# Optimization experiments

Measured on AMD Instinct MI355X. Metric: run time of the kernel, lower is better.

Reference implementation:

```python
import jax, jax.numpy as jnp
import numpy as np

B, N, D = 32, 65536, 16
M, H, OUT = 32, 64, 3  # m_model_output, hidden width, i_model output


def setup_inputs() -> dict:
    key = jax.random.key(0)
    ks = jax.random.split(key, 5)
    s = lambda fan_in: 1.0 / np.sqrt(fan_in)
    return {
        "inputs": jax.random.normal(ks[0], (B, N, D), dtype=jnp.float32),
        "mw1": jax.random.normal(ks[1], (D, H), dtype=jnp.float32) * s(D),
        "mb1": jnp.zeros((H,), dtype=jnp.float32),
        "mw2": jax.random.normal(ks[2], (H, M), dtype=jnp.float32) * s(H),
        "mb2": jnp.zeros((M,), dtype=jnp.float32),
        "iw1": jax.random.normal(ks[3], (M + 1, H), dtype=jnp.float32) * s(M + 1),
        "ib1": jnp.zeros((H,), dtype=jnp.float32),
        "iw2": jax.random.normal(ks[4], (H, OUT), dtype=jnp.float32) * s(H),
        "ib2": jnp.zeros((OUT,), dtype=jnp.float32),
    }


def reference(inputs, mw1, mb1, mw2, mb2, iw1, ib1, iw2, ib2):
    # m_model: per-node MLP producing messages [B, N, M]
    h = jax.nn.relu(jnp.einsum("bnd,dh->bnh", inputs, mw1) + mb1)
    messages = jnp.einsum("bnh,hm->bnm", h, mw2) + mb2
    # concat(messages[:j], messages[j:]) is identity -> sum over ALL nodes
    msg_sum = jnp.sum(messages, axis=1, keepdims=True)  # [B, 1, M]
    msg_sum = jnp.broadcast_to(msg_sum, (inputs.shape[0], inputs.shape[1], messages.shape[-1]))
    # append each node's last scalar feature -> [B, N, M+1]
    feat = jnp.concatenate([msg_sum, inputs[..., -1:]], axis=-1)
    # i_model: per-node MLP -> [B, N, OUT]
    g = jax.nn.relu(jnp.einsum("bnf,fh->bnh", feat, iw1) + ib1)
    out = jnp.einsum("bnh,ho->bno", g, iw2) + ib2
    return out
```

## Files before the change

### kernel.cpp

```cpp
#include <hip/hip_runtime.h>
#include <hip/hip_bf16.h>

#define Bb   32
#define Nn   65536
#define Dd   16
#define Hh   64
#define Mm   32
#define OUTn 3

#define TPB    256
#define CHUNK  256
#define NCH    8
#define SEGN   (CHUNK * NCH)
#define NWAVES ((Bb * Nn) / 512)
#define WPB    (NWAVES / Bb)
#define NSEG   65

typedef __attribute__((ext_vector_type(8)))  __bf16 bf16x8;
typedef __attribute__((ext_vector_type(4)))  __bf16 bf16x4;
typedef __attribute__((ext_vector_type(16))) float  f32x16;
typedef __attribute__((ext_vector_type(4)))  float  f32x4;

static __device__ inline void split_bf(float w, __bf16& hi, __bf16& lo) {
    hi = (__bf16)w;
    lo = (__bf16)(w - (float)hi);
}

typedef const __attribute__((address_space(1))) unsigned int gu32;
typedef __attribute__((address_space(3))) unsigned int lu32;
static __device__ __forceinline__ void gld16(const float* g, float* l) {
    __builtin_amdgcn_global_load_lds((gu32*)g, (lu32*)l, 16, 0, 0);
}

__global__ __launch_bounds__(TPB) void k_mphase(
    const float* __restrict__ in, const float* __restrict__ mw1,
    const float* __restrict__ mb1, float* __restrict__ partials,
    __bf16* __restrict__ xlast)
{
    __shared__ float lds[2][CHUNK * Dd];

    const int tid  = threadIdx.x;
    const int lane = tid & 63;
    const int w    = tid >> 6;
    const int l31  = lane & 31;
    const int half = lane >> 5;
    const size_t blk0 = (size_t)blockIdx.x * SEGN;

    bf16x8 bhiA, bloA, bhiB, bloB;
#pragma unroll
    for (int e = 0; e < 8; ++e) {
        const int k = 8 * half + e;
        __bf16 h, l;
        split_bf(mw1[k * Hh + l31], h, l);        bhiA[e] = h; bloA[e] = l;
        split_bf(mw1[k * Hh + 32 + l31], h, l);   bhiB[e] = h; bloB[e] = l;
    }
    const float biasA = mb1[l31];
    const float biasB = mb1[32 + l31];

    float hsumA = 0.f, hsumB = 0.f;

    auto stage = [&](int bf, int c) {
        const float* src = in + (blk0 + (size_t)c * CHUNK + tid) * Dd;
#pragma unroll
        for (int q = 0; q < 4; ++q)
            gld16(src + q * 4, &lds[bf][(size_t)(q * CHUNK) * 4 + (size_t)w * 256]);
    };

    int cur = 0;
    stage(0, 0);
    __syncthreads();

#pragma unroll 1
    for (int c = 0; c < NCH; ++c) {
        if (c + 1 < NCH) stage(cur ^ 1, c + 1);

#pragma unroll
        for (int T = 0; T < 2; ++T) {
            const int nb = w * 64 + T * 32 + l31;
            const int q0 = half * 2;
            f32x4 v0 = *(const f32x4*)&lds[cur][(size_t)(q0 * CHUNK + nb) * 4];
            f32x4 v1 = *(const f32x4*)&lds[cur][(size_t)((q0 + 1) * CHUNK + nb) * 4];

            bf16x8 a;
            a[0] = (__bf16)v0[0]; a[1] = (__bf16)v0[1];
            a[2] = (__bf16)v0[2]; a[3] = (__bf16)v0[3];
            a[4] = (__bf16)v1[0]; a[5] = (__bf16)v1[1];
            a[6] = (__bf16)v1[2]; a[7] = (__bf16)v1[3];

            f32x16 z{};
            f32x16 accA = __builtin_amdgcn_mfma_f32_32x32x16_bf16(a, bloA, z, 0, 0, 0);
            accA        = __builtin_amdgcn_mfma_f32_32x32x16_bf16(a, bhiA, accA, 0, 0, 0);
            f32x16 accB = __builtin_amdgcn_mfma_f32_32x32x16_bf16(a, bloB, z, 0, 0, 0);
            accB        = __builtin_amdgcn_mfma_f32_32x32x16_bf16(a, bhiB, accB, 0, 0, 0);

#pragma unroll
            for (int r = 0; r < 16; ++r) {
                accA[r] = fmaxf(accA[r] + biasA, 0.f);
                accB[r] = fmaxf(accB[r] + biasB, 0.f);
            }
#pragma unroll
            for (int st = 8; st >= 1; st >>= 1)
#pragma unroll
                for (int r = 0; r < st; ++r) {
                    accA[r] += accA[r + st];
                    accB[r] += accB[r + st];
                }
            hsumA += accA[0]; hsumB += accB[0];

            float x15 = __shfl_xor(v1[3], 32, 64);
            if (lane < 32)
                xlast[blk0 + (size_t)c * CHUNK + w * 64 + T * 32 + lane] = (__bf16)x15;
        }

        __syncthreads();
        cur ^= 1;
    }

    hsumA += __shfl_xor(hsumA, 32, 64);
    hsumB += __shfl_xor(hsumB, 32, 64);
    const int wid = blockIdx.x * 4 + w;
    partials[(size_t)wid * Hh + lane] = (lane < 32) ? hsumA : hsumB;
}

__global__ __launch_bounds__(256) void k_combine(
    const float* __restrict__ partials,
    const float* __restrict__ mw2, const float* __restrict__ mb2,
    const float* __restrict__ iw1, const float* __restrict__ ib1,
    const float* __restrict__ iw2, const float* __restrict__ ib2,
    float* __restrict__ knotsG, float* __restrict__ segG)
{
    __shared__ float red[4][Hh];
    __shared__ float sHs[Hh], sMs[Mm], sBase[Hh], sW[Hh], sKn[Hh], sSort[Hh];
    __shared__ float sIw2[Hh * OUTn];
    const int b = blockIdx.x;
    const int t = threadIdx.x;
    const int h = t & 63, slice = t >> 6;

    float s = 0.f;
    const float* p = partials + ((size_t)b * WPB + slice * 32) * Hh + h;
#pragma unroll 8
    for (int ww = 0; ww < 32; ++ww) s += p[(size_t)ww * Hh];
    red[slice][h] = s;
    for (int i = t; i < Hh * OUTn; i += 256) sIw2[i] = iw2[i];
    __syncthreads();

    if (t < Hh) sHs[t] = red[0][t] + red[1][t] + red[2][t] + red[3][t];
    __syncthreads();

    if (t < Mm) {
        float v = (float)Nn * mb2[t];
        for (int hh = 0; hh < Hh; ++hh) v = fmaf(sHs[hh], mw2[hh * Mm + t], v);
        sMs[t] = v;
    }
    __syncthreads();

    if (t < Hh) {
        float bs = ib1[t];
        for (int m = 0; m < Mm; ++m) bs = fmaf(sMs[m], iw1[m * Hh + t], bs);
        float w = iw1[Mm * Hh + t];
        sBase[t] = bs; sW[t] = w;
        float k = (w != 0.f) ? (-bs / w) : 1e15f;
        if (!(fabsf(k) < 1e15f)) k = 1e15f;
        sKn[t] = k;
    }
    __syncthreads();

    if (t < Hh) {
        float k = sKn[t];
        int r = 0;
        for (int j = 0; j < Hh; ++j) {
            float kj = sKn[j];
            r += (kj < k || (kj == k && j < t)) ? 1 : 0;
        }
        sSort[r] = k;
    }
    __syncthreads();

    if (t < Hh) knotsG[(size_t)b * Hh + t] = sSort[t];
    if (t < NSEG) {
        float lo = (t == 0)  ? sSort[0] - 1.0f      : sSort[t - 1];
        float hi = (t == Hh) ? sSort[Hh - 1] + 1.0f : sSort[t];
        float m  = 0.5f * lo + 0.5f * hi;
        float A0 = ib2[0], A1 = ib2[1], A2 = ib2[2], B0 = 0.f, B1 = 0.f, B2 = 0.f;
        for (int hh = 0; hh < Hh; ++hh) {
            float bs = sBase[hh], w = sW[hh];
            if (fmaf(w, m, bs) > 0.f) {
                A0 = fmaf(bs, sIw2[hh * 3 + 0], A0);
                A1 = fmaf(bs, sIw2[hh * 3 + 1], A1);
                A2 = fmaf(bs, sIw2[hh * 3 + 2], A2);
                B0 = fmaf(w,  sIw2[hh * 3 + 0], B0);
                B1 = fmaf(w,  sIw2[hh * 3 + 1], B1);
                B2 = fmaf(w,  sIw2[hh * 3 + 2], B2);
            }
        }
        float* sg = segG + (size_t)b * 6 * NSEG;
        sg[0 * NSEG + t] = A0; sg[1 * NSEG + t] = A1; sg[2 * NSEG + t] = A2;
        sg[3 * NSEG + t] = B0; sg[4 * NSEG + t] = B1; sg[5 * NSEG + t] = B2;
    }
}

__global__ __launch_bounds__(TPB) void k_iphase(
    const __bf16* __restrict__ xl, const float* __restrict__ knotsG,
    const float* __restrict__ segG, float* __restrict__ out)
{
    __shared__ __align__(16) float sK[Hh];
    __shared__ float sT[6 * NSEG];
    const int t = threadIdx.x;
    const int b = blockIdx.x >> 6;

    if (t < Hh) sK[t] = knotsG[(size_t)b * Hh + t];
    for (int i = t; i < 6 * NSEG; i += TPB) sT[i] = segG[(size_t)b * 6 * NSEG + i];
    __syncthreads();

    const size_t n0 = ((size_t)blockIdx.x * TPB + t) * 4;
    bf16x4 xv = *(const bf16x4*)(xl + n0);
    float o[12];
#pragma unroll
    for (int i = 0; i < 4; ++i) {
        const float x = (float)xv[i];
        int pos = 0;
#pragma unroll
        for (int st = 32; st >= 1; st >>= 1)
            pos += (sK[pos + st - 1] < x) ? st : 0;
        pos += (sK[pos] < x) ? 1 : 0;
        o[3 * i + 0] = fmaf(sT[3 * NSEG + pos], x, sT[0 * NSEG + pos]);
        o[3 * i + 1] = fmaf(sT[4 * NSEG + pos], x, sT[1 * NSEG + pos]);
        o[3 * i + 2] = fmaf(sT[5 * NSEG + pos], x, sT[2 * NSEG + pos]);
    }
    f32x4* po = (f32x4*)(out + n0 * 3);
    po[0] = f32x4{o[0], o[1], o[2],  o[3]};
    po[1] = f32x4{o[4], o[5], o[6],  o[7]};
    po[2] = f32x4{o[8], o[9], o[10], o[11]};
}

extern "C" void kernel_launch(void* const* d_in, const int* in_sizes, int n_in,
                              void* d_out, int out_size, void* d_ws, size_t ws_size,
                              hipStream_t stream) {
    const float* in  = (const float*)d_in[0];
    const float* mw1 = (const float*)d_in[1];
    const float* mb1 = (const float*)d_in[2];
    const float* mw2 = (const float*)d_in[3];
    const float* mb2 = (const float*)d_in[4];
    const float* iw1 = (const float*)d_in[5];
    const float* ib1 = (const float*)d_in[6];
    const float* iw2 = (const float*)d_in[7];
    const float* ib2 = (const float*)d_in[8];
    float* out = (float*)d_out;

    char* ws = (char*)d_ws;
    const size_t PART_SZ = (size_t)NWAVES * Hh * sizeof(float);
    float*  partials = (float*)(ws);
    float*  knotsG   = (float*)(ws + PART_SZ);
    float*  segG     = (float*)(ws + PART_SZ + 8192);
    __bf16* xl       = (__bf16*)(ws + PART_SZ + 131072);

    const int nblocks = (Bb * Nn) / SEGN;
    hipLaunchKernelGGL(k_mphase, dim3(nblocks), dim3(TPB), 0, stream,
                       in, mw1, mb1, partials, xl);
    hipLaunchKernelGGL(k_combine, dim3(Bb), dim3(256), 0, stream,
                       partials, mw2, mb2, iw1, ib1, iw2, ib2, knotsG, segG);
    hipLaunchKernelGGL(k_iphase, dim3((Bb * Nn) / (TPB * 4)), dim3(TPB), 0, stream,
                       xl, knotsG, segG, out);
}
```

Measured before the change: 52.28 us.

## Fuse three phases into one cooperative kernel with grid syncs

Replaces the three separate launches (m-phase reduction, per-batch combine, i-phase evaluation) with a single cooperative kernel that uses two grid-wide syncs. Each of 256 blocks of 512 threads now processes 8192 nodes and keeps the last-feature values in LDS, so they no longer round-trip through global memory. This removes two launch boundaries and the global write and read of the intermediate bf16 array. In exchange the grid is limited to co-resident blocks, only 32 blocks do the combine step while the rest wait at the grid barrier, and the larger block and LDS footprint lowers occupancy.

```diff
diff --git a/kernel.cpp b/kernel.cpp
--- a/kernel.cpp
+++ b/kernel.cpp
@@ -1,5 +1,8 @@
 #include <hip/hip_runtime.h>
 #include <hip/hip_bf16.h>
+#include <hip/hip_cooperative_groups.h>
+
+namespace cg = cooperative_groups;
 
 #define Bb   32
 #define Nn   65536
@@ -8,12 +11,13 @@
 #define Mm   32
 #define OUTn 3
 
-#define TPB    256
+#define TPB    512
 #define CHUNK  256
-#define NCH    8
+#define NCH    32
 #define SEGN   (CHUNK * NCH)
-#define NWAVES ((Bb * Nn) / 512)
-#define WPB    (NWAVES / Bb)
+#define NBLK   ((Bb * Nn) / SEGN)
+#define NWAVES (NBLK * 8)
+#define WPBATCH (NWAVES / Bb)
 #define NSEG   65
 
 typedef __attribute__((ext_vector_type(8)))  __bf16 bf16x8;
@@ -32,12 +36,20 @@
     __builtin_amdgcn_global_load_lds((gu32*)g, (lu32*)l, 16, 0, 0);
 }
 
-__global__ __launch_bounds__(TPB) void k_mphase(
-    const float* __restrict__ in, const float* __restrict__ mw1,
-    const float* __restrict__ mb1, float* __restrict__ partials,
-    __bf16* __restrict__ xlast)
+__global__ __launch_bounds__(TPB) void k_fused(
+    const float* __restrict__ in,
+    const float* __restrict__ mw1, const float* __restrict__ mb1,
+    const float* __restrict__ mw2, const float* __restrict__ mb2,
+    const float* __restrict__ iw1, const float* __restrict__ ib1,
+    const float* __restrict__ iw2, const float* __restrict__ ib2,
+    float* __restrict__ out,
+    float* __restrict__ partials, float* __restrict__ knotsG,
+    float* __restrict__ segG)
 {
-    __shared__ float lds[2][CHUNK * Dd];
+    cg::grid_group grid = cg::this_grid();
+
+    __shared__ float  lds[2][CHUNK * Dd];
+    __shared__ __bf16 xs[SEGN];
 
     const int tid  = threadIdx.x;
     const int lane = tid & 63;
@@ -46,37 +58,40 @@
     const int half = lane >> 5;
     const size_t blk0 = (size_t)blockIdx.x * SEGN;
 
-    bf16x8 bhiA, bloA, bhiB, bloB;
-#pragma unroll
-    for (int e = 0; e < 8; ++e) {
-        const int k = 8 * half + e;
-        __bf16 h, l;
-        split_bf(mw1[k * Hh + l31], h, l);        bhiA[e] = h; bloA[e] = l;
-        split_bf(mw1[k * Hh + 32 + l31], h, l);   bhiB[e] = h; bloB[e] = l;
-    }
-    const float biasA = mb1[l31];
-    const float biasB = mb1[32 + l31];
-
-    float hsumA = 0.f, hsumB = 0.f;
-
-    auto stage = [&](int bf, int c) {
-        const float* src = in + (blk0 + (size_t)c * CHUNK + tid) * Dd;
-#pragma unroll
-        for (int q = 0; q < 4; ++q)
-            gld16(src + q * 4, &lds[bf][(size_t)(q * CHUNK) * 4 + (size_t)w * 256]);
-    };
-
-    int cur = 0;
-    stage(0, 0);
-    __syncthreads();
+    {
+        bf16x8 bhiA, bloA, bhiB, bloB;
+#pragma unroll
+        for (int e = 0; e < 8; ++e) {
+            const int k = 8 * half + e;
+            __bf16 h, l;
+            split_bf(mw1[k * Hh + l31], h, l);        bhiA[e] = h; bloA[e] = l;
+            split_bf(mw1[k * Hh + 32 + l31], h, l);   bhiB[e] = h; bloB[e] = l;
+        }
+        const float biasA = mb1[l31];
+        const float biasB = mb1[32 + l31];
+
+        float hsumA = 0.f, hsumB = 0.f;
+
+        auto stage = [&](int bf, int c) {
+            const float* base = in + (blk0 + (size_t)c * CHUNK) * Dd;
+#pragma unroll
+            for (int gi = 0; gi < 2; ++gi) {
+                const int g  = tid + gi * TPB;
+                const int q  = g >> 8;
+                const int nd = g & 255;
+                gld16(base + (size_t)nd * Dd + q * 4, &lds[bf][(size_t)g * 4]);
+            }
+        };
+
+        int cur = 0;
+        stage(0, 0);
+        __syncthreads();
 
 #pragma unroll 1
-    for (int c = 0; c < NCH; ++c) {
-        if (c + 1 < NCH) stage(cur ^ 1, c + 1);
-
-#pragma unroll
-        for (int T = 0; T < 2; ++T) {
-            const int nb = w * 64 + T * 32 + l31;
+        for (int c = 0; c < NCH; ++c) {
+            if (c + 1 < NCH) stage(cur ^ 1, c + 1);
+
+            const int nb = w * 32 + l31;
             const int q0 = half * 2;
             f32x4 v0 = *(const f32x4*)&lds[cur][(size_t)(q0 * CHUNK + nb) * 4];
             f32x4 v1 = *(const f32x4*)&lds[cur][(size_t)((q0 + 1) * CHUNK + nb) * 4];
@@ -109,128 +124,138 @@
 
             float x15 = __shfl_xor(v1[3], 32, 64);
             if (lane < 32)
-                xlast[blk0 + (size_t)c * CHUNK + w * 64 + T * 32 + lane] = (__bf16)x15;
-        }
-
-        __syncthreads();
-        cur ^= 1;
+                xs[c * CHUNK + w * 32 + lane] = (__bf16)x15;
+
+            __syncthreads();
+            cur ^= 1;
+        }
+
+        hsumA += __shfl_xor(hsumA, 32, 64);
+        hsumB += __shfl_xor(hsumB, 32, 64);
+        const int wid = blockIdx.x * 8 + w;
+        partials[(size_t)wid * Hh + lane] = (lane < 32) ? hsumA : hsumB;
     }
 
-    hsumA += __shfl_xor(hsumA, 32, 64);
-    hsumB += __shfl_xor(hsumB, 32, 64);
-    const int wid = blockIdx.x * 4 + w;
-    partials[(size_t)wid * Hh + lane] = (lane < 32) ? hsumA : hsumB;
-}
-
-__global__ __launch_bounds__(256) void k_combine(
-    const float* __restrict__ partials,
-    const float* __restrict__ mw2, const float* __restrict__ mb2,
-    const float* __restrict__ iw1, const float* __restrict__ ib1,
-    const float* __restrict__ iw2, const float* __restrict__ ib2,
-    float* __restrict__ knotsG, float* __restrict__ segG)
-{
-    __shared__ float red[4][Hh];
-    __shared__ float sHs[Hh], sMs[Mm], sBase[Hh], sW[Hh], sKn[Hh], sSort[Hh];
-    __shared__ float sIw2[Hh * OUTn];
-    const int b = blockIdx.x;
-    const int t = threadIdx.x;
-    const int h = t & 63, slice = t >> 6;
-
-    float s = 0.f;
-    const float* p = partials + ((size_t)b * WPB + slice * 32) * Hh + h;
-#pragma unroll 8
-    for (int ww = 0; ww < 32; ++ww) s += p[(size_t)ww * Hh];
-    red[slice][h] = s;
-    for (int i = t; i < Hh * OUTn; i += 256) sIw2[i] = iw2[i];
-    __syncthreads();
-
-    if (t < Hh) sHs[t] = red[0][t] + red[1][t] + red[2][t] + red[3][t];
-    __syncthreads();
-
-    if (t < Mm) {
-        float v = (float)Nn * mb2[t];
-        for (int hh = 0; hh < Hh; ++hh) v = fmaf(sHs[hh], mw2[hh * Mm + t], v);
-        sMs[t] = v;
+    grid.sync();
+
+    if (blockIdx.x < Bb) {
+        float* ov    = &lds[0][0];
+        float* sHs   = ov;
+        float* sMs   = ov + 64;
+        float* sBase = ov + 96;
+        float* sW    = ov + 160;
+        float* sKn   = ov + 224;
+        float* sSort = ov + 288;
+        float* sIw2  = ov + 352;
+        float (*red)[Hh] = (float (*)[Hh])(ov + 544);
+
+        const int b = blockIdx.x;
+        const int t = tid;
+        const int h = t & 63, slice = t >> 6;
+
+        float s = 0.f;
+        const float* p = partials + ((size_t)b * WPBATCH + slice * 8) * Hh + h;
+#pragma unroll
+        for (int ww = 0; ww < 8; ++ww) s += p[(size_t)ww * Hh];
+        red[slice][h] = s;
+        for (int i = t; i < Hh * OUTn; i += TPB) sIw2[i] = iw2[i];
+        __syncthreads();
+
+        if (t < Hh) {
+            float v = 0.f;
+#pragma unroll
+            for (int sl = 0; sl < 8; ++sl) v += red[sl][t];
+            sHs[t] = v;
+        }
+        __syncthreads();
+
+        if (t < Mm) {
+            float v = (float)Nn * mb2[t];
+            for (int hh = 0; hh < Hh; ++hh) v = fmaf(sHs[hh], mw2[hh * Mm + t], v);
+            sMs[t] = v;
+        }
+        __syncthreads();
+
+        if (t < Hh) {
+            float bs = ib1[t];
+            for (int m = 0; m < Mm; ++m) bs = fmaf(sMs[m], iw1[m * Hh + t], bs);
+            float wv = iw1[Mm * Hh + t];
+            sBase[t] = bs; sW[t] = wv;
+            float k = (wv != 0.f) ? (-bs / wv) : 1e15f;
+            if (!(fabsf(k) < 1e15f)) k = 1e15f;
+            sKn[t] = k;
+        }
+        __syncthreads();
+
+        if (t < Hh) {
+            float k = sKn[t];
+            int r = 0;
+            for (int j = 0; j < Hh; ++j) {
+                float kj = sKn[j];
+                r += (kj < k || (kj == k && j < t)) ? 1 : 0;
+            }
+            sSort[r] = k;
+        }
+        __syncthreads();
+
+        if (t < Hh) knotsG[(size_t)b * Hh + t] = sSort[t];
+        if (t < NSEG) {
+            float lo = (t == 0)  ? sSort[0] - 1.0f      : sSort[t - 1];
+            float hi = (t == Hh) ? sSort[Hh - 1] + 1.0f : sSort[t];
+            float m  = 0.5f * lo + 0.5f * hi;
+            float A0 = ib2[0], A1 = ib2[1], A2 = ib2[2], B0 = 0.f, B1 = 0.f, B2 = 0.f;
+            for (int hh = 0; hh < Hh; ++hh) {
+                float bs = sBase[hh], wv = sW[hh];
+                if (fmaf(wv, m, bs) > 0.f) {
+                    A0 = fmaf(bs, sIw2[hh * 3 + 0], A0);
+                    A1 = fmaf(bs, sIw2[hh * 3 + 1], A1);
+                    A2 = fmaf(bs, sIw2[hh * 3 + 2], A2);
+                    B0 = fmaf(wv, sIw2[hh * 3 + 0], B0);
+                    B1 = fmaf(wv, sIw2[hh * 3 + 1], B1);
+                    B2 = fmaf(wv, sIw2[hh * 3 + 2], B2);
+                }
+            }
+            float* sg = segG + (size_t)b * 6 * NSEG;
+            sg[0 * NSEG + t] = A0; sg[1 * NSEG + t] = A1; sg[2 * NSEG + t] = A2;
+            sg[3 * NSEG + t] = B0; sg[4 * NSEG + t] = B1; sg[5 * NSEG + t] = B2;
+        }
     }
-    __syncthreads();
-
-    if (t < Hh) {
-        float bs = ib1[t];
-        for (int m = 0; m < Mm; ++m) bs = fmaf(sMs[m], iw1[m * Hh + t], bs);
-        float w = iw1[Mm * Hh + t];
-        sBase[t] = bs; sW[t] = w;
-        float k = (w != 0.f) ? (-bs / w) : 1e15f;
-        if (!(fabsf(k) < 1e15f)) k = 1e15f;
-        sKn[t] = k;
+
+    grid.sync();
+
+    {
+        const int bt = blockIdx.x >> 3;
+        float* ov = &lds[0][0];
+        float* sK = ov;
+        float* sT = ov + Hh;
+
+        if (tid < Hh) sK[tid] = knotsG[(size_t)bt * Hh + tid];
+        for (int i = tid; i < 6 * NSEG; i += TPB) sT[i] = segG[(size_t)bt * 6 * NSEG + i];
+        __syncthreads();
+
+#pragma unroll 1
+        for (int k = 0; k < SEGN / (TPB * 4); ++k) {
+            const int ln4 = (k * TPB + tid) * 4;
+            bf16x4 xv = *(const bf16x4*)(xs + ln4);
+            float o[12];
+#pragma unroll
+            for (int i = 0; i < 4; ++i) {
+                const float x = (float)xv[i];
+                int pos = 0;
+#pragma unroll
+                for (int st = 32; st >= 1; st >>= 1)
+                    pos += (sK[pos + st - 1] < x) ? st : 0;
+                pos += (sK[pos] < x) ? 1 : 0;
+                o[3 * i + 0] = fmaf(sT[3 * NSEG + pos], x, sT[0 * NSEG + pos]);
+                o[3 * i + 1] = fmaf(sT[4 * NSEG + pos], x, sT[1 * NSEG + pos]);
+                o[3 * i + 2] = fmaf(sT[5 * NSEG + pos], x, sT[2 * NSEG + pos]);
+            }
+            f32x4* po = (f32x4*)(out + (blk0 + (size_t)ln4) * 3);
+            po[0] = f32x4{o[0], o[1], o[2],  o[3]};
+            po[1] = f32x4{o[4], o[5], o[6],  o[7]};
+            po[2] = f32x4{o[8], o[9], o[10], o[11]};
+        }
     }
-    __syncthreads();
-
-    if (t < Hh) {
-        float k = sKn[t];
-        int r = 0;
-        for (int j = 0; j < Hh; ++j) {
-            float kj = sKn[j];
-            r += (kj < k || (kj == k && j < t)) ? 1 : 0;
-        }
-        sSort[r] = k;
-    }
-    __syncthreads();
-
-    if (t < Hh) knotsG[(size_t)b * Hh + t] = sSort[t];
-    if (t < NSEG) {
-        float lo = (t == 0)  ? sSort[0] - 1.0f      : sSort[t - 1];
-        float hi = (t == Hh) ? sSort[Hh - 1] + 1.0f : sSort[t];
-        float m  = 0.5f * lo + 0.5f * hi;
-        float A0 = ib2[0], A1 = ib2[1], A2 = ib2[2], B0 = 0.f, B1 = 0.f, B2 = 0.f;
-        for (int hh = 0; hh < Hh; ++hh) {
-            float bs = sBase[hh], w = sW[hh];
-            if (fmaf(w, m, bs) > 0.f) {
-                A0 = fmaf(bs, sIw2[hh * 3 + 0], A0);
-                A1 = fmaf(bs, sIw2[hh * 3 + 1], A1);
-                A2 = fmaf(bs, sIw2[hh * 3 + 2], A2);
-                B0 = fmaf(w,  sIw2[hh * 3 + 0], B0);
-                B1 = fmaf(w,  sIw2[hh * 3 + 1], B1);
-                B2 = fmaf(w,  sIw2[hh * 3 + 2], B2);
-            }
-        }
-        float* sg = segG + (size_t)b * 6 * NSEG;
-        sg[0 * NSEG + t] = A0; sg[1 * NSEG + t] = A1; sg[2 * NSEG + t] = A2;
-        sg[3 * NSEG + t] = B0; sg[4 * NSEG + t] = B1; sg[5 * NSEG + t] = B2;
-    }
-}
-
-__global__ __launch_bounds__(TPB) void k_iphase(
-    const __bf16* __restrict__ xl, const float* __restrict__ knotsG,
-    const float* __restrict__ segG, float* __restrict__ out)
-{
-    __shared__ __align__(16) float sK[Hh];
-    __shared__ float sT[6 * NSEG];
-    const int t = threadIdx.x;
-    const int b = blockIdx.x >> 6;
-
-    if (t < Hh) sK[t] = knotsG[(size_t)b * Hh + t];
-    for (int i = t; i < 6 * NSEG; i += TPB) sT[i] = segG[(size_t)b * 6 * NSEG + i];
-    __syncthreads();
-
-    const size_t n0 = ((size_t)blockIdx.x * TPB + t) * 4;
-    bf16x4 xv = *(const bf16x4*)(xl + n0);
-    float o[12];
-#pragma unroll
-    for (int i = 0; i < 4; ++i) {
-        const float x = (float)xv[i];
-        int pos = 0;
-#pragma unroll
-        for (int st = 32; st >= 1; st >>= 1)
-            pos += (sK[pos + st - 1] < x) ? st : 0;
-        pos += (sK[pos] < x) ? 1 : 0;
-        o[3 * i + 0] = fmaf(sT[3 * NSEG + pos], x, sT[0 * NSEG + pos]);
-        o[3 * i + 1] = fmaf(sT[4 * NSEG + pos], x, sT[1 * NSEG + pos]);
-        o[3 * i + 2] = fmaf(sT[5 * NSEG + pos], x, sT[2 * NSEG + pos]);
-    }
-    f32x4* po = (f32x4*)(out + n0 * 3);
-    po[0] = f32x4{o[0], o[1], o[2],  o[3]};
-    po[1] = f32x4{o[4], o[5], o[6],  o[7]};
-    po[2] = f32x4{o[8], o[9], o[10], o[11]};
 }
 
 extern "C" void kernel_launch(void* const* d_in, const int* in_sizes, int n_in,
@@ -249,16 +274,15 @@
 
     char* ws = (char*)d_ws;
     const size_t PART_SZ = (size_t)NWAVES * Hh * sizeof(float);
-    float*  partials = (float*)(ws);
-    float*  knotsG   = (float*)(ws + PART_SZ);
-    float*  segG     = (float*)(ws + PART_SZ + 8192);
-    __bf16* xl       = (__bf16*)(ws + PART_SZ + 131072);
-
-    const int nblocks = (Bb * Nn) / SEGN;
-    hipLaunchKernelGGL(k_mphase, dim3(nblocks), dim3(TPB), 0, stream,
-                       in, mw1, mb1, partials, xl);
-    hipLaunchKernelGGL(k_combine, dim3(Bb), dim3(256), 0, stream,
-                       partials, mw2, mb2, iw1, ib1, iw2, ib2, knotsG, segG);
-    hipLaunchKernelGGL(k_iphase, dim3((Bb * Nn) / (TPB * 4)), dim3(TPB), 0, stream,
-                       xl, knotsG, segG, out);
-}
+    float* partials = (float*)(ws);
+    float* knotsG   = (float*)(ws + PART_SZ);
+    float* segG     = (float*)(ws + PART_SZ + 8192);
+
+    void* args[] = {
+        (void*)&in, (void*)&mw1, (void*)&mb1, (void*)&mw2, (void*)&mb2,
+        (void*)&iw1, (void*)&ib1, (void*)&iw2, (void*)&ib2, (void*)&out,
+        (void*)&partials, (void*)&knotsG, (void*)&segG
+    };
+    hipLaunchCooperativeKernel((const void*)k_fused, dim3(NBLK), dim3(TPB),
+                               args, 0, stream);
+}
```

Result: slower. 123.5 us (+136.2%).

## Fuse combine kernel into i-phase, recomputing per-batch tables in each block

Applied to the files above, without the earlier changes.

Removes the separate per-batch combine kernel and folds its work into the i-phase kernel. Each of 512 blocks now reduces the partial sums, computes the knots and piecewise-linear segment tables for its batch in shared memory, and then processes 4096 nodes in a loop. This eliminates one kernel launch, the serial 32-block combine stage, and the global round trip for knots and segments. The cost is that the small serial combine work is repeated 16 times per batch, which lengthens each block's prologue before its streaming work can start.

```diff
diff --git a/kernel.cpp b/kernel.cpp
--- a/kernel.cpp
+++ b/kernel.cpp
@@ -16,6 +16,10 @@
 #define WPB    (NWAVES / Bb)
 #define NSEG   65
 
+#define IBLK   512
+#define INODES ((Bb * Nn) / IBLK)
+#define IBPB   (IBLK / Bb)
+
 typedef __attribute__((ext_vector_type(8)))  __bf16 bf16x8;
 typedef __attribute__((ext_vector_type(4)))  __bf16 bf16x4;
 typedef __attribute__((ext_vector_type(16))) float  f32x16;
@@ -57,8 +61,6 @@
     const float biasA = mb1[l31];
     const float biasB = mb1[32 + l31];
 
-    float hsumA = 0.f, hsumB = 0.f;
-
     auto stage = [&](int bf, int c) {
         const float* src = in + (blk0 + (size_t)c * CHUNK + tid) * Dd;
 #pragma unroll
@@ -66,6 +68,7 @@
             gld16(src + q * 4, &lds[bf][(size_t)(q * CHUNK) * 4 + (size_t)w * 256]);
     };
 
+    float hsumA = 0.f, hsumB = 0.f;
     int cur = 0;
     stage(0, 0);
     __syncthreads();
@@ -122,115 +125,116 @@
     partials[(size_t)wid * Hh + lane] = (lane < 32) ? hsumA : hsumB;
 }
 
-__global__ __launch_bounds__(256) void k_combine(
-    const float* __restrict__ partials,
+__global__ __launch_bounds__(TPB) void k_iphase2(
+    const __bf16* __restrict__ xl, const float* __restrict__ partials,
     const float* __restrict__ mw2, const float* __restrict__ mb2,
     const float* __restrict__ iw1, const float* __restrict__ ib1,
     const float* __restrict__ iw2, const float* __restrict__ ib2,
-    float* __restrict__ knotsG, float* __restrict__ segG)
-{
-    __shared__ float red[4][Hh];
-    __shared__ float sHs[Hh], sMs[Mm], sBase[Hh], sW[Hh], sKn[Hh], sSort[Hh];
-    __shared__ float sIw2[Hh * OUTn];
-    const int b = blockIdx.x;
-    const int t = threadIdx.x;
-    const int h = t & 63, slice = t >> 6;
-
-    float s = 0.f;
-    const float* p = partials + ((size_t)b * WPB + slice * 32) * Hh + h;
-#pragma unroll 8
-    for (int ww = 0; ww < 32; ++ww) s += p[(size_t)ww * Hh];
-    red[slice][h] = s;
-    for (int i = t; i < Hh * OUTn; i += 256) sIw2[i] = iw2[i];
-    __syncthreads();
-
-    if (t < Hh) sHs[t] = red[0][t] + red[1][t] + red[2][t] + red[3][t];
-    __syncthreads();
-
-    if (t < Mm) {
-        float v = (float)Nn * mb2[t];
-        for (int hh = 0; hh < Hh; ++hh) v = fmaf(sHs[hh], mw2[hh * Mm + t], v);
-        sMs[t] = v;
-    }
-    __syncthreads();
-
-    if (t < Hh) {
-        float bs = ib1[t];
-        for (int m = 0; m < Mm; ++m) bs = fmaf(sMs[m], iw1[m * Hh + t], bs);
-        float w = iw1[Mm * Hh + t];
-        sBase[t] = bs; sW[t] = w;
-        float k = (w != 0.f) ? (-bs / w) : 1e15f;
-        if (!(fabsf(k) < 1e15f)) k = 1e15f;
-        sKn[t] = k;
-    }
-    __syncthreads();
-
-    if (t < Hh) {
-        float k = sKn[t];
-        int r = 0;
-        for (int j = 0; j < Hh; ++j) {
-            float kj = sKn[j];
-            r += (kj < k || (kj == k && j < t)) ? 1 : 0;
-        }
-        sSort[r] = k;
-    }
-    __syncthreads();
-
-    if (t < Hh) knotsG[(size_t)b * Hh + t] = sSort[t];
-    if (t < NSEG) {
-        float lo = (t == 0)  ? sSort[0] - 1.0f      : sSort[t - 1];
-        float hi = (t == Hh) ? sSort[Hh - 1] + 1.0f : sSort[t];
-        float m  = 0.5f * lo + 0.5f * hi;
-        float A0 = ib2[0], A1 = ib2[1], A2 = ib2[2], B0 = 0.f, B1 = 0.f, B2 = 0.f;
-        for (int hh = 0; hh < Hh; ++hh) {
-            float bs = sBase[hh], w = sW[hh];
-            if (fmaf(w, m, bs) > 0.f) {
-                A0 = fmaf(bs, sIw2[hh * 3 + 0], A0);
-                A1 = fmaf(bs, sIw2[hh * 3 + 1], A1);
-                A2 = fmaf(bs, sIw2[hh * 3 + 2], A2);
-                B0 = fmaf(w,  sIw2[hh * 3 + 0], B0);
-                B1 = fmaf(w,  sIw2[hh * 3 + 1], B1);
-                B2 = fmaf(w,  sIw2[hh * 3 + 2], B2);
-            }
-        }
-        float* sg = segG + (size_t)b * 6 * NSEG;
-        sg[0 * NSEG + t] = A0; sg[1 * NSEG + t] = A1; sg[2 * NSEG + t] = A2;
-        sg[3 * NSEG + t] = B0; sg[4 * NSEG + t] = B1; sg[5 * NSEG + t] = B2;
-    }
-}
-
-__global__ __launch_bounds__(TPB) void k_iphase(
-    const __bf16* __restrict__ xl, const float* __restrict__ knotsG,
-    const float* __restrict__ segG, float* __restrict__ out)
+    float* __restrict__ out)
 {
     __shared__ __align__(16) float sK[Hh];
     __shared__ float sT[6 * NSEG];
+    __shared__ float scr[544];
+    __shared__ float red[4][Hh];
+
     const int t = threadIdx.x;
-    const int b = blockIdx.x >> 6;
-
-    if (t < Hh) sK[t] = knotsG[(size_t)b * Hh + t];
-    for (int i = t; i < 6 * NSEG; i += TPB) sT[i] = segG[(size_t)b * 6 * NSEG + i];
-    __syncthreads();
-
-    const size_t n0 = ((size_t)blockIdx.x * TPB + t) * 4;
-    bf16x4 xv = *(const bf16x4*)(xl + n0);
-    float o[12];
-#pragma unroll
-    for (int i = 0; i < 4; ++i) {
-        const float x = (float)xv[i];
-        int pos = 0;
-#pragma unroll
-        for (int st = 32; st >= 1; st >>= 1)
-            pos += (sK[pos + st - 1] < x) ? st : 0;
-        pos += (sK[pos] < x) ? 1 : 0;
-        o[3 * i + 0] = fmaf(sT[3 * NSEG + pos], x, sT[0 * NSEG + pos]);
-        o[3 * i + 1] = fmaf(sT[4 * NSEG + pos], x, sT[1 * NSEG + pos]);
-        o[3 * i + 2] = fmaf(sT[5 * NSEG + pos], x, sT[2 * NSEG + pos]);
-    }
-    f32x4* po = (f32x4*)(out + n0 * 3);
-    po[0] = f32x4{o[0], o[1], o[2],  o[3]};
-    po[1] = f32x4{o[4], o[5], o[6],  o[7]};
-    po[2] = f32x4{o[8], o[9], o[10], o[11]};
+    const int b = blockIdx.x / IBPB;
+
+    {
+        const int h = t & 63, slice = t >> 6;
+        float s = 0.f;
+        const float* p = partials + ((size_t)b * WPB + slice * 32) * Hh + h;
+#pragma unroll 8
+        for (int ww = 0; ww < 32; ++ww) s += p[(size_t)ww * Hh];
+        red[slice][h] = s;
+        for (int i = t; i < Hh * OUTn; i += TPB) scr[352 + i] = iw2[i];
+        __syncthreads();
+
+        float* sHs  = scr;
+        float* sMs  = scr + 64;
+        float* sBase= scr + 96;
+        float* sW   = scr + 160;
+        float* sKn  = scr + 224;
+        float* sIw2 = scr + 352;
+
+        if (t < Hh) sHs[t] = red[0][t] + red[1][t] + red[2][t] + red[3][t];
+        __syncthreads();
+
+        if (t < Mm) {
+            float v = (float)Nn * mb2[t];
+            for (int hh = 0; hh < Hh; ++hh) v = fmaf(sHs[hh], mw2[hh * Mm + t], v);
+            sMs[t] = v;
+        }
+        __syncthreads();
+
+        if (t < Hh) {
+            float bs = ib1[t];
+            for (int m = 0; m < Mm; ++m) bs = fmaf(sMs[m], iw1[m * Hh + t], bs);
+            float wv = iw1[Mm * Hh + t];
+            sBase[t] = bs; sW[t] = wv;
+            float kk = (wv != 0.f) ? (-bs / wv) : 1e15f;
+            if (!(fabsf(kk) < 1e15f)) kk = 1e15f;
+            sKn[t] = kk;
+        }
+        __syncthreads();
+
+        if (t < Hh) {
+            float kk = sKn[t];
+            int r = 0;
+            for (int j = 0; j < Hh; ++j) {
+                float kj = sKn[j];
+                r += (kj < kk || (kj == kk && j < t)) ? 1 : 0;
+            }
+            sK[r] = kk;
+        }
+        __syncthreads();
+
+        if (t < NSEG) {
+            float lo = (t == 0)  ? sK[0] - 1.0f      : sK[t - 1];
+            float hi = (t == Hh) ? sK[Hh - 1] + 1.0f : sK[t];
+            float m  = 0.5f * lo + 0.5f * hi;
+            float A0 = ib2[0], A1 = ib2[1], A2 = ib2[2];
+            float B0 = 0.f, B1 = 0.f, B2 = 0.f;
+            for (int hh = 0; hh < Hh; ++hh) {
+                float bs = sBase[hh], wv = sW[hh];
+                if (fmaf(wv, m, bs) > 0.f) {
+                    A0 = fmaf(bs, sIw2[hh * 3 + 0], A0);
+                    A1 = fmaf(bs, sIw2[hh * 3 + 1], A1);
+                    A2 = fmaf(bs, sIw2[hh * 3 + 2], A2);
+                    B0 = fmaf(wv, sIw2[hh * 3 + 0], B0);
+                    B1 = fmaf(wv, sIw2[hh * 3 + 1], B1);
+                    B2 = fmaf(wv, sIw2[hh * 3 + 2], B2);
+                }
+            }
+            sT[0 * NSEG + t] = A0; sT[1 * NSEG + t] = A1; sT[2 * NSEG + t] = A2;
+            sT[3 * NSEG + t] = B0; sT[4 * NSEG + t] = B1; sT[5 * NSEG + t] = B2;
+        }
+        __syncthreads();
+    }
+
+    const size_t base = (size_t)blockIdx.x * INODES;
+#pragma unroll
+    for (int k = 0; k < INODES / (TPB * 4); ++k) {
+        const size_t n0 = base + (size_t)(k * TPB + t) * 4;
+        bf16x4 xv = *(const bf16x4*)(xl + n0);
+        float o[12];
+#pragma unroll
+        for (int i = 0; i < 4; ++i) {
+            const float x = (float)xv[i];
+            int pos = 0;
+#pragma unroll
+            for (int st = 32; st >= 1; st >>= 1)
+                pos += (sK[pos + st - 1] < x) ? st : 0;
+            pos += (sK[pos] < x) ? 1 : 0;
+            o[3 * i + 0] = fmaf(sT[3 * NSEG + pos], x, sT[0 * NSEG + pos]);
+            o[3 * i + 1] = fmaf(sT[4 * NSEG + pos], x, sT[1 * NSEG + pos]);
+            o[3 * i + 2] = fmaf(sT[5 * NSEG + pos], x, sT[2 * NSEG + pos]);
+        }
+        f32x4* po = (f32x4*)(out + n0 * 3);
+        po[0] = f32x4{o[0], o[1], o[2],  o[3]};
+        po[1] = f32x4{o[4], o[5], o[6],  o[7]};
+        po[2] = f32x4{o[8], o[9], o[10], o[11]};
+    }
 }
 
 extern "C" void kernel_launch(void* const* d_in, const int* in_sizes, int n_in,
@@ -250,15 +254,11 @@
     char* ws = (char*)d_ws;
     const size_t PART_SZ = (size_t)NWAVES * Hh * sizeof(float);
     float*  partials = (float*)(ws);
-    float*  knotsG   = (float*)(ws + PART_SZ);
-    float*  segG     = (float*)(ws + PART_SZ + 8192);
     __bf16* xl       = (__bf16*)(ws + PART_SZ + 131072);
 
     const int nblocks = (Bb * Nn) / SEGN;
     hipLaunchKernelGGL(k_mphase, dim3(nblocks), dim3(TPB), 0, stream,
                        in, mw1, mb1, partials, xl);
-    hipLaunchKernelGGL(k_combine, dim3(Bb), dim3(256), 0, stream,
-                       partials, mw2, mb2, iw1, ib1, iw2, ib2, knotsG, segG);
-    hipLaunchKernelGGL(k_iphase, dim3((Bb * Nn) / (TPB * 4)), dim3(TPB), 0, stream,
-                       xl, knotsG, segG, out);
-}
+    hipLaunchKernelGGL(k_iphase2, dim3(IBLK), dim3(TPB), 0, stream,
+                       xl, partials, mw2, mb2, iw1, ib1, iw2, ib2, out);
+}
```

After: 50.86 us. 1.03x faster.
